# Kernel tuning notes

Hardware: AMD Instinct MI355X
Metric: run time of the kernel (lower is better)

The kernel has to match this reference:

```python
import jax, jax.numpy as jnp
import numpy as np

LN_EPS = 1e-5

def layernorm(x, w, b):
    mu = jnp.mean(x, axis=-1, keepdims=True)
    var = jnp.mean(jnp.square(x - mu), axis=-1, keepdims=True)
    return (x - mu) * jax.lax.rsqrt(var + LN_EPS) * w + b

def l2_normalize(x, eps=1e-12):
    n = jnp.sqrt(jnp.sum(jnp.square(x), axis=-1, keepdims=True))
    return x / jnp.maximum(n, eps)

def setup_inputs() -> dict:
    key = jax.random.key(0)
    k1, k2 = jax.random.split(key)
    B, D, Npix = 8, 64, 32768
    K, P = 19, 5
    return {
        "base_feature": jax.random.normal(k1, (B, D, Npix), dtype=jnp.float32),
        "means": jax.random.normal(k2, (K, P, D), dtype=jnp.float32) * 0.02,  # trunc_normal_(std=0.02)
        "diagonal": jnp.ones((K, P, D), dtype=jnp.float32),
        "feat_w": jnp.ones((D,), dtype=jnp.float32),
        "feat_b": jnp.zeros((D,), dtype=jnp.float32),
        "mask_w": jnp.ones((K,), dtype=jnp.float32),
        "mask_b": jnp.zeros((K,), dtype=jnp.float32),
    }

def gmm_log_prob(x, mu, scale):
    # x: [N, D]; mu, scale: [KP, D]  (MultivariateNormalDiag with scale_diag=scale)
    # log p = -0.5 * sum(((x-mu)/s)^2) - sum(log s) - 0.5*D*log(2*pi)
    D = x.shape[-1]
    inv2 = 1.0 / jnp.square(scale)                      # [KP, D]
    quad = (jnp.square(x) @ inv2.T                       # [N, KP]
            - 2.0 * (x @ (mu * inv2).T)
            + jnp.sum(jnp.square(mu) * inv2, axis=-1))
    log_norm = jnp.sum(jnp.log(scale), axis=-1) + 0.5 * D * jnp.log(2.0 * jnp.pi)
    return -0.5 * quad - log_norm                        # [N, KP]

def reference(base_feature, means, diagonal, feat_w, feat_b, mask_w, mask_b):
    B, D, Npix = base_feature.shape
    K, P, _ = means.shape
    # 'b c n -> (b n) c'
    _c = jnp.transpose(base_feature, (0, 2, 1)).reshape(B * Npix, D)
    _c = layernorm(_c, feat_w, feat_b)
    _c = l2_normalize(_c)
    means_n = l2_normalize(means)                        # means.data.copy_(l2_normalize(means))
    logp = gmm_log_prob(_c, means_n.reshape(K * P, D), diagonal.reshape(K * P, D))
    final_probs = logp.reshape(-1, K, P)                 # [(b n), K, P]
    _m_prob = jnp.max(final_probs, axis=-1)              # amax over components -> [(b n), K]
    out_seg = layernorm(_m_prob, mask_w, mask_b)         # mask_norm
    # '(b n) k -> b k n'
    out_seg = jnp.transpose(out_seg.reshape(B, Npix, K), (0, 2, 1))
    return out_seg
```

## Files before the change

kernel.cpp:

```cpp
#include <hip/hip_runtime.h>
#include <math.h>

#define BB    8
#define DD    64
#define NPIX  32768
#define KK    19
#define PP    5
#define NROW  112

typedef _Float16 half8  __attribute__((ext_vector_type(8)));
typedef __fp16   half2t __attribute__((ext_vector_type(2)));
typedef float    f32x4  __attribute__((ext_vector_type(4)));

union H8 { half8 v; half2t p[4]; };

__global__ __launch_bounds__(64) void gmm_prep(
        const float* __restrict__ means, const float* __restrict__ diag,
        const float* __restrict__ feat_w, const float* __restrict__ feat_b,
        _Float16* __restrict__ Ch, float* __restrict__ cst,
        float* __restrict__ scal) {
    const int R = blockIdx.x;
    const int d = threadIdx.x;
    if (R == NROW) {
        float w = feat_w[d], b = feat_b[d];
        float s0 = w * w, s1 = w * b, s2 = b * b;
        #pragma unroll
        for (int off = 32; off; off >>= 1) {
            s0 += __shfl_xor(s0, off);
            s1 += __shfl_xor(s1, off);
            s2 += __shfl_xor(s2, off);
        }
        if (d == 0) { scal[0] = s0; scal[1] = s1; scal[2] = s2; }
        return;
    }
    int g, p; bool valid;
    if (R < 80)      { g = 4 * (R >> 4) + ((R >> 2) & 3); p = R & 3; valid = (g < KK); }
    else if (R < 96) { g = 4 * ((R - 80) & 3) + ((R - 80) >> 2); p = 4; valid = true; }
    else             { g = 16 + ((R - 96) >> 2); p = 4; valid = ((R & 3) == 0) && (g < KK); }
    if (valid) {
        const int j = 5 * g + p;
        float mu = means[j * DD + d];
        float sc = diag[j * DD + d];
        float ss = mu * mu;
        #pragma unroll
        for (int off = 32; off; off >>= 1) ss += __shfl_xor(ss, off);
        float inv = 1.f / fmaxf(sqrtf(ss), 1e-12f);
        float mn = mu * inv;
        float i2 = 1.f / (sc * sc);
        Ch[R * 128 + 2 * d]     = (_Float16)(mn * i2);
        Ch[R * 128 + 2 * d + 1] = (_Float16)(-0.5f * i2);
        float c1 = mn * mn * i2;
        float c2 = logf(sc);
        #pragma unroll
        for (int off = 32; off; off >>= 1) {
            c1 += __shfl_xor(c1, off);
            c2 += __shfl_xor(c2, off);
        }
        if (d == 0) cst[R] = -0.5f * c1 - c2;
    } else {
        Ch[R * 128 + 2 * d]     = (_Float16)0.f;
        Ch[R * 128 + 2 * d + 1] = (_Float16)0.f;
        if (d == 0) cst[R] = 0.f;
    }
}

#define DO_TILE(T, MERGE) {                                                   \
    const _Float16* ab = cb + (size_t)((T) * 16 * 128);                       \
    const half8 A0 = *(const half8*)(ab);                                     \
    const half8 A1 = *(const half8*)(ab + 32);                                \
    const half8 A2 = *(const half8*)(ab + 64);                                \
    const half8 A3 = *(const half8*)(ab + 96);                                \
    const float4 cc = *(const float4*)(cst + 16 * (T) + 4 * q);               \
    f32x4 a0 = {0.f, 0.f, 0.f, 0.f}, a1 = {0.f, 0.f, 0.f, 0.f};               \
    a0 = __builtin_amdgcn_mfma_f32_16x16x32_f16(A0, Uh[0][0].v, a0, 0, 0, 0); \
    a1 = __builtin_amdgcn_mfma_f32_16x16x32_f16(A0, Uh[1][0].v, a1, 0, 0, 0); \
    a0 = __builtin_amdgcn_mfma_f32_16x16x32_f16(A1, Uh[0][1].v, a0, 0, 0, 0); \
    a1 = __builtin_amdgcn_mfma_f32_16x16x32_f16(A1, Uh[1][1].v, a1, 0, 0, 0); \
    a0 = __builtin_amdgcn_mfma_f32_16x16x32_f16(A2, Uh[0][2].v, a0, 0, 0, 0); \
    a1 = __builtin_amdgcn_mfma_f32_16x16x32_f16(A2, Uh[1][2].v, a1, 0, 0, 0); \
    a0 = __builtin_amdgcn_mfma_f32_16x16x32_f16(A3, Uh[0][3].v, a0, 0, 0, 0); \
    a1 = __builtin_amdgcn_mfma_f32_16x16x32_f16(A3, Uh[1][3].v, a1, 0, 0, 0); \
    a0 = __builtin_amdgcn_mfma_f32_16x16x32_f16(A0, Ul[0][0].v, a0, 0, 0, 0); \
    a1 = __builtin_amdgcn_mfma_f32_16x16x32_f16(A0, Ul[1][0].v, a1, 0, 0, 0); \
    a0 = __builtin_amdgcn_mfma_f32_16x16x32_f16(A1, Ul[0][1].v, a0, 0, 0, 0); \
    a1 = __builtin_amdgcn_mfma_f32_16x16x32_f16(A1, Ul[1][1].v, a1, 0, 0, 0); \
    a0 = __builtin_amdgcn_mfma_f32_16x16x32_f16(A2, Ul[0][2].v, a0, 0, 0, 0); \
    a1 = __builtin_amdgcn_mfma_f32_16x16x32_f16(A2, Ul[1][2].v, a1, 0, 0, 0); \
    a0 = __builtin_amdgcn_mfma_f32_16x16x32_f16(A3, Ul[0][3].v, a0, 0, 0, 0); \
    a1 = __builtin_amdgcn_mfma_f32_16x16x32_f16(A3, Ul[1][3].v, a1, 0, 0, 0); \
    MERGE                                                                     \
}

#define MERGE_SLOT(T)                                                              \
    m0[T] = fmaxf(fmaxf(a0[0] + cc.x, a0[1] + cc.y), fmaxf(a0[2] + cc.z, a0[3] + cc.w)); \
    m1[T] = fmaxf(fmaxf(a1[0] + cc.x, a1[1] + cc.y), fmaxf(a1[2] + cc.z, a1[3] + cc.w));

#define MERGE_C4A                                                \
    m0[0] = fmaxf(m0[0], a0[0] + cc.x);                          \
    m0[1] = fmaxf(m0[1], a0[1] + cc.y);                          \
    m0[2] = fmaxf(m0[2], a0[2] + cc.z);                          \
    m0[3] = fmaxf(m0[3], a0[3] + cc.w);                          \
    m1[0] = fmaxf(m1[0], a1[0] + cc.x);                          \
    m1[1] = fmaxf(m1[1], a1[1] + cc.y);                          \
    m1[2] = fmaxf(m1[2], a1[2] + cc.z);                          \
    m1[3] = fmaxf(m1[3], a1[3] + cc.w);

#define MERGE_C4B                                                \
    m0[4] = fmaxf(m0[4], a0[0] + cc.x);                          \
    m1[4] = fmaxf(m1[4], a1[0] + cc.x);

__global__ __launch_bounds__(256, 4) void gmm_main(
        const float* __restrict__ bf,
        const float* __restrict__ feat_w, const float* __restrict__ feat_b,
        const float* __restrict__ mask_w, const float* __restrict__ mask_b,
        const _Float16* __restrict__ Ch, const float* __restrict__ cst,
        const float* __restrict__ scal, float* __restrict__ out) {
    const int tid  = threadIdx.x;
    const int w    = tid >> 6;
    const int lane = tid & 63;
    const int m15  = lane & 15;
    const int q    = lane >> 4;
    const int bidx = blockIdx.x;
    const int b    = bidx >> 8;
    const int n0   = ((bidx & 255) << 7) + (w << 5);

    const float* xp = bf + (size_t)b * (DD * NPIX) + n0 + m15;
    float xs0[16], xs1[16];
    #pragma unroll
    for (int ks = 0; ks < 4; ++ks)
        #pragma unroll
        for (int i = 0; i < 4; ++i) {
            const size_t off = (size_t)(ks * 16 + q * 4 + i) * NPIX;
            xs0[ks * 4 + i] = xp[off];
            xs1[ks * 4 + i] = xp[off + 16];
        }

    float4 wv[4], bv[4];
    #pragma unroll
    for (int ks = 0; ks < 4; ++ks) {
        wv[ks] = *(const float4*)(feat_w + ks * 16 + q * 4);
        bv[ks] = *(const float4*)(feat_b + ks * 16 + q * 4);
    }

    float S1a = 0.f, S2a = 0.f, S3a = 0.f, S4a = 0.f, S5a = 0.f;
    float S1b = 0.f, S2b = 0.f, S3b = 0.f, S4b = 0.f, S5b = 0.f;
    #pragma unroll
    for (int ks = 0; ks < 4; ++ks)
        #pragma unroll
        for (int i = 0; i < 4; ++i) {
            float wd = ((const float*)&wv[ks])[i];
            float bd = ((const float*)&bv[ks])[i];
            float xa = xs0[ks * 4 + i], xb = xs1[ks * 4 + i];
            float ta = wd * xa, tb = wd * xb;
            S1a += xa; S2a = fmaf(xa, xa, S2a); S3a = fmaf(ta, ta, S3a);
            S4a = fmaf(ta, wd, S4a); S5a = fmaf(ta, bd, S5a);
            S1b += xb; S2b = fmaf(xb, xb, S2b); S3b = fmaf(tb, tb, S3b);
            S4b = fmaf(tb, wd, S4b); S5b = fmaf(tb, bd, S5b);
        }
    S1a += __shfl_xor(S1a, 16); S1a += __shfl_xor(S1a, 32);
    S2a += __shfl_xor(S2a, 16); S2a += __shfl_xor(S2a, 32);
    S3a += __shfl_xor(S3a, 16); S3a += __shfl_xor(S3a, 32);
    S4a += __shfl_xor(S4a, 16); S4a += __shfl_xor(S4a, 32);
    S5a += __shfl_xor(S5a, 16); S5a += __shfl_xor(S5a, 32);
    S1b += __shfl_xor(S1b, 16); S1b += __shfl_xor(S1b, 32);
    S2b += __shfl_xor(S2b, 16); S2b += __shfl_xor(S2b, 32);
    S3b += __shfl_xor(S3b, 16); S3b += __shfl_xor(S3b, 32);
    S4b += __shfl_xor(S4b, 16); S4b += __shfl_xor(S4b, 32);
    S5b += __shfl_xor(S5b, 16); S5b += __shfl_xor(S5b, 32);

    const float W2 = scal[0], WB = scal[1], B2 = scal[2];
    float al0, e0, f0, al1, e1, f1;
    {
        float mu  = S1a * (1.f / 64.f);
        float var = fmaxf(S2a * (1.f / 64.f) - mu * mu, 0.f);
        float r   = rsqrtf(var + 1e-5f);
        float Sy2 = r * r * (S3a - 2.f * mu * S4a + mu * mu * W2)
                  + 2.f * r * (S5a - mu * WB) + B2;
        float invn = 1.f / fmaxf(sqrtf(fmaxf(Sy2, 0.f)), 1e-12f);
        al0 = invn * r; e0 = invn; f0 = -al0 * mu;
    }
    {
        float mu  = S1b * (1.f / 64.f);
        float var = fmaxf(S2b * (1.f / 64.f) - mu * mu, 0.f);
        float r   = rsqrtf(var + 1e-5f);
        float Sy2 = r * r * (S3b - 2.f * mu * S4b + mu * mu * W2)
                  + 2.f * r * (S5b - mu * WB) + B2;
        float invn = 1.f / fmaxf(sqrtf(fmaxf(Sy2, 0.f)), 1e-12f);
        al1 = invn * r; e1 = invn; f1 = -al1 * mu;
    }

    H8 Uh[2][4], Ul[2][4];
    #pragma unroll
    for (int ks = 0; ks < 4; ++ks) {
        #pragma unroll
        for (int i = 0; i < 4; ++i) {
            float wd = ((const float*)&wv[ks])[i];
            float bd = ((const float*)&bv[ks])[i];
            float c0 = fmaf(f0, wd, e0 * bd);
            float c1 = fmaf(f1, wd, e1 * bd);
            float u0 = fmaf(al0, wd * xs0[ks * 4 + i], c0);
            float u1 = fmaf(al1, wd * xs1[ks * 4 + i], c1);
            float q0 = u0 * u0, q1 = u1 * u1;
            half2t h0 = __builtin_amdgcn_cvt_pkrtz(u0, q0);
            half2t h1 = __builtin_amdgcn_cvt_pkrtz(u1, q1);
            half2t l0 = __builtin_amdgcn_cvt_pkrtz(u0 - (float)h0[0], q0 - (float)h0[1]);
            half2t l1 = __builtin_amdgcn_cvt_pkrtz(u1 - (float)h1[0], q1 - (float)h1[1]);
            Uh[0][ks].p[i] = h0; Ul[0][ks].p[i] = l0;
            Uh[1][ks].p[i] = h1; Ul[1][ks].p[i] = l1;
        }
    }

    const _Float16* cb = Ch + (size_t)m15 * 128 + q * 8;
    float m0[5], m1[5];
    DO_TILE(0, MERGE_SLOT(0))
    DO_TILE(1, MERGE_SLOT(1))
    DO_TILE(2, MERGE_SLOT(2))
    DO_TILE(3, MERGE_SLOT(3))
    DO_TILE(4, MERGE_SLOT(4))
    DO_TILE(5, MERGE_C4A)
    DO_TILE(6, MERGE_C4B)

    const bool v4 = (q < 3);
    float S0 = m0[0] + m0[1] + m0[2] + m0[3] + (v4 ? m0[4] : 0.f);
    float S1 = m1[0] + m1[1] + m1[2] + m1[3] + (v4 ? m1[4] : 0.f);
    S0 += __shfl_xor(S0, 16); S0 += __shfl_xor(S0, 32);
    S1 += __shfl_xor(S1, 16); S1 += __shfl_xor(S1, 32);
    const float mu0 = S0 * (1.f / 19.f), mu1 = S1 * (1.f / 19.f);
    float V0, V1;
    {
        float d0 = m0[0] - mu0, d1 = m0[1] - mu0, d2 = m0[2] - mu0;
        float d3 = m0[3] - mu0, d4 = m0[4] - mu0;
        V0 = d0 * d0 + d1 * d1 + d2 * d2 + d3 * d3 + (v4 ? d4 * d4 : 0.f);
    }
    {
        float d0 = m1[0] - mu1, d1 = m1[1] - mu1, d2 = m1[2] - mu1;
        float d3 = m1[3] - mu1, d4 = m1[4] - mu1;
        V1 = d0 * d0 + d1 * d1 + d2 * d2 + d3 * d3 + (v4 ? d4 * d4 : 0.f);
    }
    V0 += __shfl_xor(V0, 16); V0 += __shfl_xor(V0, 32);
    V1 += __shfl_xor(V1, 16); V1 += __shfl_xor(V1, 32);
    const float r0 = rsqrtf(V0 * (1.f / 19.f) + 1e-5f);
    const float r1 = rsqrtf(V1 * (1.f / 19.f) + 1e-5f);

    float* op = out + (size_t)b * (KK * NPIX) + n0 + m15;
    #pragma unroll
    for (int t = 0; t < 5; ++t) {
        const int k = 4 * t + q;
        if (t < 4 || v4) {
            const float mw = mask_w[k], mb = mask_b[k];
            op[(size_t)k * NPIX]      = (m0[t] - mu0) * r0 * mw + mb;
            op[(size_t)k * NPIX + 16] = (m1[t] - mu1) * r1 * mw + mb;
        }
    }
}

extern "C" void kernel_launch(void* const* d_in, const int* in_sizes, int n_in,
                              void* d_out, int out_size, void* d_ws, size_t ws_size,
                              hipStream_t stream) {
    const float* base_feature = (const float*)d_in[0];
    const float* means        = (const float*)d_in[1];
    const float* diagonal     = (const float*)d_in[2];
    const float* feat_w       = (const float*)d_in[3];
    const float* feat_b       = (const float*)d_in[4];
    const float* mask_w       = (const float*)d_in[5];
    const float* mask_b       = (const float*)d_in[6];
    float* out = (float*)d_out;

    _Float16* Ch = (_Float16*)d_ws;
    float* cst   = (float*)(Ch + NROW * 128);
    float* scal  = cst + NROW;

    gmm_prep<<<NROW + 1, 64, 0, stream>>>(means, diagonal, feat_w, feat_b, Ch, cst, scal);

    gmm_main<<<(BB * NPIX) / 128, 256, 0, stream>>>(
        base_feature, feat_w, feat_b, mask_w, mask_b, Ch, cst, scal, out);
}
```

Baseline: 140.8 us.

## Stage input and output through LDS for float4 global access; prefetch MFMA tiles

Input features are now loaded with float4 global reads into a per-wave shared-memory tile and read back in the MFMA layout. Outputs are likewise staged in shared memory and written as float4 rows. The cluster-coefficient tiles are software-prefetched one tile ahead inside a rolled loop. The aim is to cut the number of global memory transactions from scalar loads and stores and to hide coefficient-load latency, at the cost of 36 KB of LDS per block, which may limit occupancy, plus two block barriers.

```diff
diff --git a/kernel.cpp b/kernel.cpp
--- a/kernel.cpp
+++ b/kernel.cpp
@@ -7,6 +7,7 @@
 #define KK    19
 #define PP    5
 #define NROW  112
+#define LPS   36
 
 typedef _Float16 half8  __attribute__((ext_vector_type(8)));
 typedef __fp16   half2t __attribute__((ext_vector_type(2)));
@@ -64,57 +65,14 @@
     }
 }
 
-#define DO_TILE(T, MERGE) {                                                   \
-    const _Float16* ab = cb + (size_t)((T) * 16 * 128);                       \
-    const half8 A0 = *(const half8*)(ab);                                     \
-    const half8 A1 = *(const half8*)(ab + 32);                                \
-    const half8 A2 = *(const half8*)(ab + 64);                                \
-    const half8 A3 = *(const half8*)(ab + 96);                                \
-    const float4 cc = *(const float4*)(cst + 16 * (T) + 4 * q);               \
-    f32x4 a0 = {0.f, 0.f, 0.f, 0.f}, a1 = {0.f, 0.f, 0.f, 0.f};               \
-    a0 = __builtin_amdgcn_mfma_f32_16x16x32_f16(A0, Uh[0][0].v, a0, 0, 0, 0); \
-    a1 = __builtin_amdgcn_mfma_f32_16x16x32_f16(A0, Uh[1][0].v, a1, 0, 0, 0); \
-    a0 = __builtin_amdgcn_mfma_f32_16x16x32_f16(A1, Uh[0][1].v, a0, 0, 0, 0); \
-    a1 = __builtin_amdgcn_mfma_f32_16x16x32_f16(A1, Uh[1][1].v, a1, 0, 0, 0); \
-    a0 = __builtin_amdgcn_mfma_f32_16x16x32_f16(A2, Uh[0][2].v, a0, 0, 0, 0); \
-    a1 = __builtin_amdgcn_mfma_f32_16x16x32_f16(A2, Uh[1][2].v, a1, 0, 0, 0); \
-    a0 = __builtin_amdgcn_mfma_f32_16x16x32_f16(A3, Uh[0][3].v, a0, 0, 0, 0); \
-    a1 = __builtin_amdgcn_mfma_f32_16x16x32_f16(A3, Uh[1][3].v, a1, 0, 0, 0); \
-    a0 = __builtin_amdgcn_mfma_f32_16x16x32_f16(A0, Ul[0][0].v, a0, 0, 0, 0); \
-    a1 = __builtin_amdgcn_mfma_f32_16x16x32_f16(A0, Ul[1][0].v, a1, 0, 0, 0); \
-    a0 = __builtin_amdgcn_mfma_f32_16x16x32_f16(A1, Ul[0][1].v, a0, 0, 0, 0); \
-    a1 = __builtin_amdgcn_mfma_f32_16x16x32_f16(A1, Ul[1][1].v, a1, 0, 0, 0); \
-    a0 = __builtin_amdgcn_mfma_f32_16x16x32_f16(A2, Ul[0][2].v, a0, 0, 0, 0); \
-    a1 = __builtin_amdgcn_mfma_f32_16x16x32_f16(A2, Ul[1][2].v, a1, 0, 0, 0); \
-    a0 = __builtin_amdgcn_mfma_f32_16x16x32_f16(A3, Ul[0][3].v, a0, 0, 0, 0); \
-    a1 = __builtin_amdgcn_mfma_f32_16x16x32_f16(A3, Ul[1][3].v, a1, 0, 0, 0); \
-    MERGE                                                                     \
-}
-
-#define MERGE_SLOT(T)                                                              \
-    m0[T] = fmaxf(fmaxf(a0[0] + cc.x, a0[1] + cc.y), fmaxf(a0[2] + cc.z, a0[3] + cc.w)); \
-    m1[T] = fmaxf(fmaxf(a1[0] + cc.x, a1[1] + cc.y), fmaxf(a1[2] + cc.z, a1[3] + cc.w));
-
-#define MERGE_C4A                                                \
-    m0[0] = fmaxf(m0[0], a0[0] + cc.x);                          \
-    m0[1] = fmaxf(m0[1], a0[1] + cc.y);                          \
-    m0[2] = fmaxf(m0[2], a0[2] + cc.z);                          \
-    m0[3] = fmaxf(m0[3], a0[3] + cc.w);                          \
-    m1[0] = fmaxf(m1[0], a1[0] + cc.x);                          \
-    m1[1] = fmaxf(m1[1], a1[1] + cc.y);                          \
-    m1[2] = fmaxf(m1[2], a1[2] + cc.z);                          \
-    m1[3] = fmaxf(m1[3], a1[3] + cc.w);
-
-#define MERGE_C4B                                                \
-    m0[4] = fmaxf(m0[4], a0[0] + cc.x);                          \
-    m1[4] = fmaxf(m1[4], a1[0] + cc.x);
-
 __global__ __launch_bounds__(256, 4) void gmm_main(
         const float* __restrict__ bf,
         const float* __restrict__ feat_w, const float* __restrict__ feat_b,
         const float* __restrict__ mask_w, const float* __restrict__ mask_b,
         const _Float16* __restrict__ Ch, const float* __restrict__ cst,
         const float* __restrict__ scal, float* __restrict__ out) {
+    __shared__ float lds[4 * DD * LPS];
+
     const int tid  = threadIdx.x;
     const int w    = tid >> 6;
     const int lane = tid & 63;
@@ -123,17 +81,15 @@
     const int bidx = blockIdx.x;
     const int b    = bidx >> 8;
     const int n0   = ((bidx & 255) << 7) + (w << 5);
-
-    const float* xp = bf + (size_t)b * (DD * NPIX) + n0 + m15;
-    float xs0[16], xs1[16];
-    #pragma unroll
-    for (int ks = 0; ks < 4; ++ks)
-        #pragma unroll
-        for (int i = 0; i < 4; ++i) {
-            const size_t off = (size_t)(ks * 16 + q * 4 + i) * NPIX;
-            xs0[ks * 4 + i] = xp[off];
-            xs1[ks * 4 + i] = xp[off + 16];
-        }
+    float* lp = lds + w * (DD * LPS);
+
+    const int rr  = lane >> 3;
+    const int c4  = (lane & 7) * 4;
+    const float* xg = bf + (size_t)b * (DD * NPIX) + n0 + c4;
+    float4 xv[8];
+    #pragma unroll
+    for (int j = 0; j < 8; ++j)
+        xv[j] = *(const float4*)(xg + (size_t)(8 * j + rr) * NPIX);
 
     float4 wv[4], bv[4];
     #pragma unroll
@@ -141,6 +97,27 @@
         wv[ks] = *(const float4*)(feat_w + ks * 16 + q * 4);
         bv[ks] = *(const float4*)(feat_b + ks * 16 + q * 4);
     }
+    const _Float16* cb = Ch + (size_t)m15 * 128 + q * 8;
+    half8 Ac[4];
+    #pragma unroll
+    for (int ks = 0; ks < 4; ++ks) Ac[ks] = *(const half8*)(cb + ks * 32);
+    float4 cv = *(const float4*)(cst + 4 * q);
+
+    #pragma unroll
+    for (int j = 0; j < 8; ++j)
+        *(float4*)(lp + (8 * j + rr) * LPS + c4) = xv[j];
+
+    __syncthreads();
+
+    float xs0[16], xs1[16];
+    #pragma unroll
+    for (int ks = 0; ks < 4; ++ks)
+        #pragma unroll
+        for (int i = 0; i < 4; ++i) {
+            const float* rp = lp + (16 * ks + 4 * q + i) * LPS + m15;
+            xs0[ks * 4 + i] = rp[0];
+            xs1[ks * 4 + i] = rp[16];
+        }
 
     float S1a = 0.f, S2a = 0.f, S3a = 0.f, S4a = 0.f, S5a = 0.f;
     float S1b = 0.f, S2b = 0.f, S3b = 0.f, S4b = 0.f, S5b = 0.f;
@@ -210,15 +187,49 @@
         }
     }
 
-    const _Float16* cb = Ch + (size_t)m15 * 128 + q * 8;
     float m0[5], m1[5];
-    DO_TILE(0, MERGE_SLOT(0))
-    DO_TILE(1, MERGE_SLOT(1))
-    DO_TILE(2, MERGE_SLOT(2))
-    DO_TILE(3, MERGE_SLOT(3))
-    DO_TILE(4, MERGE_SLOT(4))
-    DO_TILE(5, MERGE_C4A)
-    DO_TILE(6, MERGE_C4B)
+    #pragma unroll
+    for (int t = 0; t < 7; ++t) {
+        half8 An[4]; float4 cn;
+        if (t < 6) {
+            const _Float16* nb = cb + (size_t)(16 * (t + 1)) * 128;
+            #pragma unroll
+            for (int ks = 0; ks < 4; ++ks) An[ks] = *(const half8*)(nb + ks * 32);
+            cn = *(const float4*)(cst + 16 * (t + 1) + 4 * q);
+        }
+        f32x4 a0 = {0.f, 0.f, 0.f, 0.f}, a1 = {0.f, 0.f, 0.f, 0.f};
+        #pragma unroll
+        for (int ks = 0; ks < 4; ++ks) {
+            a0 = __builtin_amdgcn_mfma_f32_16x16x32_f16(Ac[ks], Uh[0][ks].v, a0, 0, 0, 0);
+            a1 = __builtin_amdgcn_mfma_f32_16x16x32_f16(Ac[ks], Uh[1][ks].v, a1, 0, 0, 0);
+        }
+        #pragma unroll
+        for (int ks = 0; ks < 4; ++ks) {
+            a0 = __builtin_amdgcn_mfma_f32_16x16x32_f16(Ac[ks], Ul[0][ks].v, a0, 0, 0, 0);
+            a1 = __builtin_amdgcn_mfma_f32_16x16x32_f16(Ac[ks], Ul[1][ks].v, a1, 0, 0, 0);
+        }
+        if (t < 5) {
+            m0[t] = fmaxf(fmaxf(a0[0] + cv.x, a0[1] + cv.y), fmaxf(a0[2] + cv.z, a0[3] + cv.w));
+            m1[t] = fmaxf(fmaxf(a1[0] + cv.x, a1[1] + cv.y), fmaxf(a1[2] + cv.z, a1[3] + cv.w));
+        } else if (t == 5) {
+            m0[0] = fmaxf(m0[0], a0[0] + cv.x);
+            m0[1] = fmaxf(m0[1], a0[1] + cv.y);
+            m0[2] = fmaxf(m0[2], a0[2] + cv.z);
+            m0[3] = fmaxf(m0[3], a0[3] + cv.w);
+            m1[0] = fmaxf(m1[0], a1[0] + cv.x);
+            m1[1] = fmaxf(m1[1], a1[1] + cv.y);
+            m1[2] = fmaxf(m1[2], a1[2] + cv.z);
+            m1[3] = fmaxf(m1[3], a1[3] + cv.w);
+        } else {
+            m0[4] = fmaxf(m0[4], a0[0] + cv.x);
+            m1[4] = fmaxf(m1[4], a1[0] + cv.x);
+        }
+        if (t < 6) {
+            #pragma unroll
+            for (int ks = 0; ks < 4; ++ks) Ac[ks] = An[ks];
+            cv = cn;
+        }
+    }
 
     const bool v4 = (q < 3);
     float S0 = m0[0] + m0[1] + m0[2] + m0[3] + (v4 ? m0[4] : 0.f);
@@ -242,14 +253,26 @@
     const float r0 = rsqrtf(V0 * (1.f / 19.f) + 1e-5f);
     const float r1 = rsqrtf(V1 * (1.f / 19.f) + 1e-5f);
 
-    float* op = out + (size_t)b * (KK * NPIX) + n0 + m15;
     #pragma unroll
     for (int t = 0; t < 5; ++t) {
         const int k = 4 * t + q;
         if (t < 4 || v4) {
             const float mw = mask_w[k], mb = mask_b[k];
-            op[(size_t)k * NPIX]      = (m0[t] - mu0) * r0 * mw + mb;
-            op[(size_t)k * NPIX + 16] = (m1[t] - mu1) * r1 * mw + mb;
+            lp[k * LPS + m15]      = (m0[t] - mu0) * r0 * mw + mb;
+            lp[k * LPS + 16 + m15] = (m1[t] - mu1) * r1 * mw + mb;
+        }
+    }
+
+    __syncthreads();
+
+    float* ob = out + (size_t)b * (KK * NPIX) + n0;
+    #pragma unroll
+    for (int rnd = 0; rnd < 3; ++rnd) {
+        const int idx = rnd * 64 + lane;
+        if (idx < 152) {
+            const int k = idx >> 3, cc = (idx & 7) * 4;
+            float4 v = *(const float4*)(lp + k * LPS + cc);
+            *(float4*)(ob + (size_t)k * NPIX + cc) = v;
         }
     }
 }
```

Result: slower. 156.8 us (+11.4%).
